# Performance work log

Measured on AMD Instinct MI355X. Metric: run time of the kernel, lower is better.

Reference implementation:

```python
import jax, jax.numpy as jnp
import numpy as np

IN_FEATURES = 4096
OUT_FEATURES = 11008
PACK = 8  # int4 values per int32


def setup_inputs() -> dict:
    key = jax.random.key(0)
    k1, k2, k3, k4, k5 = jax.random.split(key, 5)
    x = jax.random.normal(k1, (1, IN_FEATURES), dtype=jnp.float32)
    # packed int4 weights: 8 nibbles per int32 word, [in/8, out]
    qweight = jax.random.randint(k2, (IN_FEATURES // PACK, OUT_FEATURES), 0, 2147483647, dtype=jnp.int32)
    # per-output-channel quant params; zeros is already zeros*scales (as in __init__)
    scales = jax.random.uniform(k3, (OUT_FEATURES,), jnp.float32, minval=0.005, maxval=0.02)
    zeros = jax.random.uniform(k4, (OUT_FEATURES,), jnp.float32, minval=0.0, maxval=0.16)
    bias = jax.random.normal(k5, (OUT_FEATURES,), dtype=jnp.float32) * 0.01
    return {"x": x, "qweight": qweight, "scales": scales, "zeros": zeros, "bias": bias}


def reference(x, qweight, scales, zeros, bias):
    # unpack 8 int4 nibbles per int32 word along the input dim
    shifts = (jnp.arange(PACK, dtype=jnp.int32) * 4)  # [8]
    q = (qweight[:, None, :] >> shifts[None, :, None]) & 0xF  # [in/8, 8, out]
    q = q.reshape(-1, qweight.shape[-1]).astype(x.dtype)       # [in, out]
    # y = x @ (q*scales - zeros) + bias, factored so the fp matvec hits q directly:
    # scales/zeros are per-output-channel so they distribute out of the contraction.
    xq = x @ q                                                 # [1, out]
    x_sum = jnp.sum(x, axis=-1, keepdims=True)                 # [1, 1]
    return xq * scales - x_sum * zeros + bias                  # [1, out]
```

## Files before the change

### kernel.cpp

```cpp
#include <hip/hip_runtime.h>

#define IN_FEATURES 4096
#define OUT_FEATURES 11008
#define KW (IN_FEATURES / 8)
#define BLOCK 256
#define O_PER_BLOCK 32
#define KG 32
#define W_PER_THREAD (KW / KG)

__global__ __launch_bounds__(BLOCK) void quant4_matvec(
    const float* __restrict__ x,
    const int* __restrict__ qw,
    const float* __restrict__ scales,
    const float* __restrict__ zeros,
    const float* __restrict__ bias,
    float* __restrict__ out)
{
    __shared__ float xs[IN_FEATURES];
    __shared__ float red[KG][O_PER_BLOCK];
    __shared__ float xsum_s[BLOCK / 64];

    const int tid = threadIdx.x;

    float xpart = 0.f;
    const float4* x4 = (const float4*)x;
    float4* xs4 = (float4*)xs;
#pragma unroll
    for (int i = 0; i < IN_FEATURES / 4 / BLOCK; ++i) {
        float4 v = x4[i * BLOCK + tid];
        xs4[i * BLOCK + tid] = v;
        xpart += v.x + v.y + v.z + v.w;
    }
#pragma unroll
    for (int off = 32; off > 0; off >>= 1)
        xpart += __shfl_down(xpart, off);
    if ((tid & 63) == 0) xsum_s[tid >> 6] = xpart;
    __syncthreads();

    const int og = tid & 7;
    const int kg = tid >> 3;
    const int o_base = blockIdx.x * O_PER_BLOCK;
    const int o4 = o_base + og * 4;

    float acc0 = 0.f, acc1 = 0.f, acc2 = 0.f, acc3 = 0.f;
#pragma unroll
    for (int w = 0; w < W_PER_THREAD; ++w) {
        const int k = w * KG + kg;
        const int4 q = *(const int4*)(qw + k * OUT_FEATURES + o4);
        const float4 xa = *(const float4*)(&xs[k * 8]);
        const float4 xb = *(const float4*)(&xs[k * 8 + 4]);
        const float xv[8] = {xa.x, xa.y, xa.z, xa.w, xb.x, xb.y, xb.z, xb.w};
        const unsigned qx = (unsigned)q.x, qy = (unsigned)q.y,
                       qz = (unsigned)q.z, qw_ = (unsigned)q.w;
#pragma unroll
        for (int n = 0; n < 8; ++n) {
            const float xvn = xv[n];
            acc0 += xvn * (float)((qx >> (4 * n)) & 0xFu);
            acc1 += xvn * (float)((qy >> (4 * n)) & 0xFu);
            acc2 += xvn * (float)((qz >> (4 * n)) & 0xFu);
            acc3 += xvn * (float)((qw_ >> (4 * n)) & 0xFu);
        }
    }

    red[kg][og * 4 + 0] = acc0;
    red[kg][og * 4 + 1] = acc1;
    red[kg][og * 4 + 2] = acc2;
    red[kg][og * 4 + 3] = acc3;
    __syncthreads();

    if (tid < O_PER_BLOCK) {
        float s = 0.f;
#pragma unroll
        for (int g = 0; g < KG; ++g) s += red[g][tid];
        const float xsum = xsum_s[0] + xsum_s[1] + xsum_s[2] + xsum_s[3];
        const int o = o_base + tid;
        out[o] = s * scales[o] - xsum * zeros[o] + bias[o];
    }
}

extern "C" void kernel_launch(void* const* d_in, const int* in_sizes, int n_in,
                              void* d_out, int out_size, void* d_ws, size_t ws_size,
                              hipStream_t stream) {
    const float* x      = (const float*)d_in[0];
    const int*   qw     = (const int*)d_in[1];
    const float* scales = (const float*)d_in[2];
    const float* zeros  = (const float*)d_in[3];
    const float* bias   = (const float*)d_in[4];
    float* out = (float*)d_out;

    const int grid = OUT_FEATURES / O_PER_BLOCK;
    quant4_matvec<<<grid, BLOCK, 0, stream>>>(x, qw, scales, zeros, bias, out);
}
```

Baseline: 80.55 us.

## Split K dimension across blocks and combine partial sums with atomics

The contraction over input features is split four ways across a second grid dimension, so the grid grows from 344 to 1376 blocks and each block stages only a quarter of x in shared memory. Partial results are reduced inside each wave with xor shuffles, across waves through a small shared buffer, and then added into the output with atomicAdd after a memset. This targets low occupancy and latency hiding on the memory-bound matvec, but adds a memset launch, atomic traffic and non-deterministic summation order.

After: 79.72 us. About the same (-1.0%).

```diff
diff --git a/kernel.cpp b/kernel.cpp
--- a/kernel.cpp
+++ b/kernel.cpp
@@ -3,12 +3,15 @@
 #define IN_FEATURES 4096
 #define OUT_FEATURES 11008
 #define KW (IN_FEATURES / 8)
+#define SPLIT 4
+#define KWB (KW / SPLIT)
 #define BLOCK 256
-#define O_PER_BLOCK 32
+#define OPB 32
 #define KG 32
-#define W_PER_THREAD (KW / KG)
+#define W (KWB / KG)
+#define NWAVE (BLOCK / 64)
 
-__global__ __launch_bounds__(BLOCK) void quant4_matvec(
+__global__ __launch_bounds__(BLOCK) void quant4_matvec_split(
     const float* __restrict__ x,
     const int* __restrict__ qw,
     const float* __restrict__ scales,
@@ -16,21 +19,18 @@
     const float* __restrict__ bias,
     float* __restrict__ out)
 {
-    __shared__ float xs[IN_FEATURES];
-    __shared__ float red[KG][O_PER_BLOCK];
-    __shared__ float xsum_s[BLOCK / 64];
+    __shared__ float xs[KWB * 8];
+    __shared__ float red[NWAVE][OPB];
+    __shared__ float xsum_s[NWAVE];
 
     const int tid = threadIdx.x;
+    const int ob  = blockIdx.x;
+    const int q   = blockIdx.y;
 
-    float xpart = 0.f;
     const float4* x4 = (const float4*)x;
-    float4* xs4 = (float4*)xs;
-#pragma unroll
-    for (int i = 0; i < IN_FEATURES / 4 / BLOCK; ++i) {
-        float4 v = x4[i * BLOCK + tid];
-        xs4[i * BLOCK + tid] = v;
-        xpart += v.x + v.y + v.z + v.w;
-    }
+    float4 v = x4[q * (KWB * 2) + tid];
+    ((float4*)xs)[tid] = v;
+    float xpart = v.x + v.y + v.z + v.w;
 #pragma unroll
     for (int off = 32; off > 0; off >>= 1)
         xpart += __shfl_down(xpart, off);
@@ -39,42 +39,57 @@
 
     const int og = tid & 7;
     const int kg = tid >> 3;
-    const int o_base = blockIdx.x * O_PER_BLOCK;
-    const int o4 = o_base + og * 4;
+    const int o4 = ob * OPB + og * 4;
 
     float acc0 = 0.f, acc1 = 0.f, acc2 = 0.f, acc3 = 0.f;
 #pragma unroll
-    for (int w = 0; w < W_PER_THREAD; ++w) {
-        const int k = w * KG + kg;
-        const int4 q = *(const int4*)(qw + k * OUT_FEATURES + o4);
-        const float4 xa = *(const float4*)(&xs[k * 8]);
-        const float4 xb = *(const float4*)(&xs[k * 8 + 4]);
+    for (int w = 0; w < W; ++w) {
+        const int kl = w * KG + kg;
+        const int krow = q * KWB + kl;
+        const int4 qv = *(const int4*)(qw + (long)krow * OUT_FEATURES + o4);
+        const float4 xa = *(const float4*)(&xs[kl * 8]);
+        const float4 xb = *(const float4*)(&xs[kl * 8 + 4]);
         const float xv[8] = {xa.x, xa.y, xa.z, xa.w, xb.x, xb.y, xb.z, xb.w};
-        const unsigned qx = (unsigned)q.x, qy = (unsigned)q.y,
-                       qz = (unsigned)q.z, qw_ = (unsigned)q.w;
+        const unsigned qx = (unsigned)qv.x, qy = (unsigned)qv.y,
+                       qz = (unsigned)qv.z, qwv = (unsigned)qv.w;
 #pragma unroll
         for (int n = 0; n < 8; ++n) {
             const float xvn = xv[n];
             acc0 += xvn * (float)((qx >> (4 * n)) & 0xFu);
             acc1 += xvn * (float)((qy >> (4 * n)) & 0xFu);
             acc2 += xvn * (float)((qz >> (4 * n)) & 0xFu);
-            acc3 += xvn * (float)((qw_ >> (4 * n)) & 0xFu);
+            acc3 += xvn * (float)((qwv >> (4 * n)) & 0xFu);
         }
     }
 
-    red[kg][og * 4 + 0] = acc0;
-    red[kg][og * 4 + 1] = acc1;
-    red[kg][og * 4 + 2] = acc2;
-    red[kg][og * 4 + 3] = acc3;
+#pragma unroll
+    for (int m = 8; m <= 32; m <<= 1) {
+        acc0 += __shfl_xor(acc0, m);
+        acc1 += __shfl_xor(acc1, m);
+        acc2 += __shfl_xor(acc2, m);
+        acc3 += __shfl_xor(acc3, m);
+    }
+    const int lane = tid & 63;
+    const int wid  = tid >> 6;
+    if (lane < 8) {
+        red[wid][lane * 4 + 0] = acc0;
+        red[wid][lane * 4 + 1] = acc1;
+        red[wid][lane * 4 + 2] = acc2;
+        red[wid][lane * 4 + 3] = acc3;
+    }
     __syncthreads();
 
-    if (tid < O_PER_BLOCK) {
+    if (tid < OPB) {
         float s = 0.f;
 #pragma unroll
-        for (int g = 0; g < KG; ++g) s += red[g][tid];
-        const float xsum = xsum_s[0] + xsum_s[1] + xsum_s[2] + xsum_s[3];
-        const int o = o_base + tid;
-        out[o] = s * scales[o] - xsum * zeros[o] + bias[o];
+        for (int g = 0; g < NWAVE; ++g) s += red[g][tid];
+        float xsumq = 0.f;
+#pragma unroll
+        for (int g = 0; g < NWAVE; ++g) xsumq += xsum_s[g];
+        const int o = ob * OPB + tid;
+        float val = s * scales[o] - xsumq * zeros[o];
+        if (q == 0) val += bias[o];
+        atomicAdd(out + o, val);
     }
 }
 
@@ -88,6 +103,8 @@
     const float* bias   = (const float*)d_in[4];
     float* out = (float*)d_out;
 
-    const int grid = OUT_FEATURES / O_PER_BLOCK;
-    quant4_matvec<<<grid, BLOCK, 0, stream>>>(x, qw, scales, zeros, bias, out);
+    hipMemsetAsync(out, 0, OUT_FEATURES * sizeof(float), stream);
+
+    dim3 grid(OUT_FEATURES / OPB, SPLIT);
+    quant4_matvec_split<<<grid, BLOCK, 0, stream>>>(x, qw, scales, zeros, bias, out);
 }
```
